# Optimization experiments

Hardware: AMD Instinct MI355X
Metric: run time of the kernel (lower is better)

Reference implementation:

```python
import jax, jax.numpy as jnp
import numpy as np

B, INPUT_DIM, OUTPUT_DIM, Z_DIM = 32, 2048, 2048, 64
NNZ = 209715


def setup_inputs() -> dict:
    key = jax.random.key(0)
    k_x, k_z, k_w, k_b = jax.random.split(key, 4)
    x = jax.random.normal(k_x, (B, INPUT_DIM), dtype=jnp.float32)
    z = jax.random.normal(k_z, (B, Z_DIM), dtype=jnp.float32)
    W_net = jax.random.normal(k_w, (Z_DIM, NNZ), dtype=jnp.float32) * 0.02
    b_net = jax.random.normal(k_b, (NNZ,), dtype=jnp.float32) * 0.02
    # unique nonzero positions of output_matrix [INPUT_DIM, OUTPUT_DIM]
    rng = np.random.default_rng(0)
    lin = rng.choice(INPUT_DIM * OUTPUT_DIM, size=NNZ, replace=False)
    in_idx = jnp.asarray(lin // OUTPUT_DIM, dtype=jnp.int32)   # rows  -> input dim
    out_idx = jnp.asarray(lin % OUTPUT_DIM, dtype=jnp.int32)   # cols  -> output dim
    return {"x": x, "z": z, "W_net": W_net, "b_net": b_net,
            "in_idx": in_idx, "out_idx": out_idx}


def reference(x, z, W_net, b_net, in_idx, out_idx):
    # hypernetwork: net(z) -> [B, NNZ] matrix entries
    mat_entity = z @ W_net + b_net                      # [B, NNZ]
    # scatter into zero-filled dense matrix: mat[:, out_idx, in_idx] = entries
    mat = jnp.zeros((x.shape[0], OUTPUT_DIM, INPUT_DIM), dtype=x.dtype)
    mat = mat.at[:, out_idx, in_idx].set(mat_entity)    # [B, O, I]
    # batched matvec
    return jnp.einsum('boi,bi->bo', mat, x)             # [B, O]
```

## Files before the change

kernel.cpp:

```cpp
#include <hip/hip_runtime.h>
#include <hip/hip_bf16.h>

#define BATCH   32
#define IN_DIM  2048
#define OUT_DIM 2048
#define ZDIM    64
#define NNZ     209715
#define CAP     160
#define TILES   ((NNZ + 15) / 16)
#define TPW     2
#define CWAVES  ((TILES + TPW - 1) / TPW)
#define CBLOCKS ((CWAVES + 3) / 4)
#define NBLK    ((NNZ + 1023) / 1024)

typedef __attribute__((ext_vector_type(8))) short bf16x8;
typedef __attribute__((ext_vector_type(4))) float f32x4;

#define OFF_XT   0
#define OFF_ZBF  262144
#define OFF_CNT  270336
#define OFF_BH   278528
#define OFF_ROW  2375680
#define OFF_E    3214592
#define B_WS_NEEDED (OFF_E + (size_t)OUT_DIM * CAP * BATCH * 2)

__device__ __forceinline__ short f2bf(float f) {
    unsigned u = __float_as_uint(f);
    u += 0x7fffu + ((u >> 16) & 1u);
    return (short)(u >> 16);
}

__global__ __launch_bounds__(1024) void hist_prep(
    const int* __restrict__ out_idx, const float* __restrict__ x,
    const float* __restrict__ z, int* __restrict__ bh,
    float* __restrict__ xT, short* __restrict__ zbf)
{
    __shared__ int lh[OUT_DIM];
    const int t = threadIdx.x, blk = blockIdx.x;
    lh[t] = 0; lh[t + 1024] = 0;
    __syncthreads();
    const int gid = blk * 1024 + t;
    if (gid < BATCH * IN_DIM) {
        const int b = gid >> 11, i = gid & 2047;
        xT[i * BATCH + b] = x[gid];
        if (gid < BATCH * ZDIM) zbf[gid] = f2bf(z[gid]);
    }
    if (gid < NNZ) atomicAdd(&lh[out_idx[gid]], 1);
    __syncthreads();
    bh[t * 256 + blk]          = lh[t];
    bh[(t + 1024) * 256 + blk] = lh[t + 1024];
}

__global__ __launch_bounds__(256) void colscan(
    int* __restrict__ bh, int* __restrict__ cnt)
{
    const int o    = blockIdx.x * 4 + (threadIdx.x >> 6);
    const int lane = threadIdx.x & 63;
    const int i0   = lane * 4;
    int4 v = *reinterpret_cast<int4*>(bh + o * 256 + i0);
    const int a = (i0 + 0 < NBLK) ? v.x : 0;
    const int b = (i0 + 1 < NBLK) ? v.y : 0;
    const int c = (i0 + 2 < NBLK) ? v.z : 0;
    const int d = (i0 + 3 < NBLK) ? v.w : 0;
    const int s1 = a + b, s2 = s1 + c, tot = s2 + d;
    int inc = tot;
    #pragma unroll
    for (int t = 1; t < 64; t <<= 1) {
        const int n = __shfl_up(inc, t);
        if (lane >= t) inc += n;
    }
    const int exc = inc - tot;
    int4 w; w.x = exc; w.y = exc + a; w.z = exc + s1; w.w = exc + s2;
    *reinterpret_cast<int4*>(bh + o * 256 + i0) = w;
    if (lane == 63) cnt[o] = inc;
}

__global__ __launch_bounds__(1024) void slot_blk(
    const int* __restrict__ out_idx, const int* __restrict__ bh,
    int* __restrict__ rowOf)
{
    __shared__ int lh[OUT_DIM];
    const int t = threadIdx.x, blk = blockIdx.x;
    lh[t] = 0; lh[t + 1024] = 0;
    __syncthreads();
    const int k = blk * 1024 + t;
    if (k < NNZ) {
        const int oi  = out_idx[k];
        const int r   = atomicAdd(&lh[oi], 1);
        const int pos = bh[oi * 256 + blk] + r;
        rowOf[k] = (pos < CAP) ? oi * CAP + pos : -1;
    }
}

__global__ __launch_bounds__(256, 4) void compute_mfma(
    const short* __restrict__ zbf, const float* __restrict__ W,
    const float* __restrict__ bn, const int* __restrict__ in_idx,
    const int* __restrict__ rowOf, const float* __restrict__ xT,
    short* __restrict__ E)
{
    const int lane = threadIdx.x & 63;
    const int m    = lane & 15;
    const int hi   = lane >> 4;
    const int wid  = blockIdx.x * 4 + (threadIdx.x >> 6);
    const int t0   = wid * TPW;
    if (t0 >= TILES) return;

    bf16x8 zf[2][2];
    #pragma unroll
    for (int bt = 0; bt < 2; ++bt)
        #pragma unroll
        for (int jt = 0; jt < 2; ++jt)
            zf[bt][jt] = *reinterpret_cast<const bf16x8*>(
                zbf + (bt * 16 + m) * ZDIM + jt * 32 + hi * 8);

    int rowL[2] = {-1, -1}, iiL[2] = {0, 0};
    float bnL[2] = {0.f, 0.f};
    #pragma unroll
    for (int tt = 0; tt < TPW; ++tt) {
        const int t = t0 + tt;
        if (t < TILES && lane < 16) {
            const int kk = t * 16 + lane;
            if (kk < NNZ) { rowL[tt] = rowOf[kk]; iiL[tt] = in_idx[kk]; bnL[tt] = bn[kk]; }
        }
    }

    float wv[2][16];
    #pragma unroll
    for (int tt = 0; tt < TPW; ++tt) {
        const int t  = (t0 + tt < TILES) ? (t0 + tt) : (TILES - 1);
        const int kA = (t * 16 + m < NNZ) ? (t * 16 + m) : (NNZ - 1);
        const float* wp = W + (size_t)(hi * 8) * NNZ + kA;
        #pragma unroll
        for (int e = 0; e < 8; ++e) wv[tt][e]     = wp[(size_t)e * NNZ];
        #pragma unroll
        for (int e = 0; e < 8; ++e) wv[tt][8 + e] = wp[(size_t)(32 + e) * NNZ];
    }

    int   row_[2][4];
    float x0_[2][4], x1_[2][4];
    #pragma unroll
    for (int tt = 0; tt < TPW; ++tt)
        #pragma unroll
        for (int r = 0; r < 4; ++r) {
            const int src = hi * 4 + r;
            row_[tt][r] = __shfl(rowL[tt], src);
            const int ii = __shfl(iiL[tt], src);
            x0_[tt][r] = xT[ii * BATCH + m];
            x1_[tt][r] = xT[ii * BATCH + 16 + m];
        }

    #pragma unroll
    for (int tt = 0; tt < TPW; ++tt) {
        union { bf16x8 v; short s[8]; } a0, a1;
        #pragma unroll
        for (int e = 0; e < 8; ++e) { a0.s[e] = f2bf(wv[tt][e]); a1.s[e] = f2bf(wv[tt][8 + e]); }

        f32x4 acc0 = {0.f, 0.f, 0.f, 0.f};
        f32x4 acc1 = {0.f, 0.f, 0.f, 0.f};
        acc0 = __builtin_amdgcn_mfma_f32_16x16x32_bf16(a0.v, zf[0][0], acc0, 0, 0, 0);
        acc0 = __builtin_amdgcn_mfma_f32_16x16x32_bf16(a1.v, zf[0][1], acc0, 0, 0, 0);
        acc1 = __builtin_amdgcn_mfma_f32_16x16x32_bf16(a0.v, zf[1][0], acc1, 0, 0, 0);
        acc1 = __builtin_amdgcn_mfma_f32_16x16x32_bf16(a1.v, zf[1][1], acc1, 0, 0, 0);

        #pragma unroll
        for (int r = 0; r < 4; ++r) {
            const int row = row_[tt][r];
            if (row >= 0) {
                const float bb = __shfl(bnL[tt], hi * 4 + r);
                short* Ep = E + (size_t)row * BATCH;
                Ep[m]      = f2bf((acc0[r] + bb) * x0_[tt][r]);
                Ep[16 + m] = f2bf((acc1[r] + bb) * x1_[tt][r]);
            }
        }
    }
}

__global__ __launch_bounds__(256) void reduce_bf16(
    const short* __restrict__ E, const int* __restrict__ cnt,
    float* __restrict__ out)
{
    const int o    = blockIdx.x * 4 + (threadIdx.x >> 6);
    const int lane = threadIdx.x & 63;
    const int r  = lane >> 2;
    const int bg = lane & 3;
    const int s = o * CAP;
    int c = cnt[o]; if (c > CAP) c = CAP;
    const int e = s + c;

    float acc[8];
    #pragma unroll
    for (int q = 0; q < 8; ++q) acc[q] = 0.f;

    for (int p = s + r; p < e; p += 16) {
        const uint4 v = *reinterpret_cast<const uint4*>(E + (size_t)p * BATCH + bg * 8);
        const unsigned u[4] = {v.x, v.y, v.z, v.w};
        #pragma unroll
        for (int q = 0; q < 4; ++q) {
            acc[2 * q]     += __uint_as_float((u[q] & 0xFFFFu) << 16);
            acc[2 * q + 1] += __uint_as_float(u[q] & 0xFFFF0000u);
        }
    }

    #pragma unroll
    for (int d = 4; d < 64; d <<= 1)
        #pragma unroll
        for (int q = 0; q < 8; ++q)
            acc[q] += __shfl_xor(acc[q], d);

    if (lane < 4) {
        #pragma unroll
        for (int q = 0; q < 8; ++q)
            out[(bg * 8 + q) * OUT_DIM + o] = acc[q];
    }
}

__global__ __launch_bounds__(256) void hyper_scatter_kernel(
    const float* __restrict__ x, const float* __restrict__ z,
    const float* __restrict__ W, const float* __restrict__ bn,
    const int* __restrict__ in_idx, const int* __restrict__ out_idx,
    float* __restrict__ out)
{
    __shared__ float zs[BATCH * ZDIM];
    const int tid = threadIdx.x;
    {
        const float4* zg  = reinterpret_cast<const float4*>(z);
        float4*       zsv = reinterpret_cast<float4*>(zs);
        zsv[tid]       = zg[tid];
        zsv[tid + 256] = zg[tid + 256];
    }
    __syncthreads();
    const int k = blockIdx.x * 256 + tid;
    if (k >= NNZ) return;
    float w[ZDIM];
    #pragma unroll
    for (int j = 0; j < ZDIM; ++j) w[j] = W[(size_t)j * NNZ + k];
    const float bk = bn[k];
    const int ii = in_idx[k], oi = out_idx[k];
    const float4* zv = reinterpret_cast<const float4*>(zs);
    #pragma unroll
    for (int b = 0; b < BATCH; ++b) {
        float e = bk;
        #pragma unroll
        for (int j4 = 0; j4 < ZDIM / 4; ++j4) {
            const float4 zz = zv[b * (ZDIM / 4) + j4];
            e = fmaf(zz.x, w[j4 * 4 + 0], e);
            e = fmaf(zz.y, w[j4 * 4 + 1], e);
            e = fmaf(zz.z, w[j4 * 4 + 2], e);
            e = fmaf(zz.w, w[j4 * 4 + 3], e);
        }
        atomicAdd(&out[b * OUT_DIM + oi], e * x[b * IN_DIM + ii]);
    }
}

extern "C" void kernel_launch(void* const* d_in, const int* in_sizes, int n_in,
                              void* d_out, int out_size, void* d_ws, size_t ws_size,
                              hipStream_t stream) {
    const float* x       = (const float*)d_in[0];
    const float* z       = (const float*)d_in[1];
    const float* W       = (const float*)d_in[2];
    const float* bn      = (const float*)d_in[3];
    const int*   in_idx  = (const int*)d_in[4];
    const int*   out_idx = (const int*)d_in[5];
    float*       out     = (float*)d_out;
    char*        ws      = (char*)d_ws;

    if (ws_size >= B_WS_NEEDED) {
        float* xT    = (float*)(ws + OFF_XT);
        short* zbf   = (short*)(ws + OFF_ZBF);
        int*   cnt   = (int*)(ws + OFF_CNT);
        int*   bh    = (int*)(ws + OFF_BH);
        int*   rowOf = (int*)(ws + OFF_ROW);
        short* E     = (short*)(ws + OFF_E);

        hist_prep<<<NBLK, 1024, 0, stream>>>(out_idx, x, z, bh, xT, zbf);
        colscan  <<<OUT_DIM / 4, 256, 0, stream>>>(bh, cnt);
        slot_blk <<<NBLK, 1024, 0, stream>>>(out_idx, bh, rowOf);
        compute_mfma<<<CBLOCKS, 256, 0, stream>>>(zbf, W, bn, in_idx, rowOf, xT, E);
        reduce_bf16 <<<OUT_DIM / 4, 256, 0, stream>>>(E, cnt, out);
    } else {
        hipMemsetAsync(out, 0, (size_t)BATCH * OUT_DIM * sizeof(float), stream);
        const int grid = (NNZ + 255) / 256;
        hyper_scatter_kernel<<<grid, 256, 0, stream>>>(x, z, W, bn, in_idx, out_idx, out);
    }
}
```

Before: 42.78 us.

## Replace histogram/scan slot assignment with global atomic slot counters in compute

Removes the three-kernel histogram, column-scan and slot-assignment pipeline and instead assigns each nonzero's bucket slot with a global atomicAdd on a per-output counter inside the MFMA compute kernel. A small prep kernel zeroes the counters alongside the x transpose and z conversion. This cuts two kernel launches and the bh/rowOf memory traffic, at the cost of contended global atomics on 2048 counters. Slot order becomes nondeterministic, which changes the bf16 summation order in the reduce.

```diff
diff --git a/kernel.cpp b/kernel.cpp
--- a/kernel.cpp
+++ b/kernel.cpp
@@ -11,17 +11,14 @@
 #define TPW     2
 #define CWAVES  ((TILES + TPW - 1) / TPW)
 #define CBLOCKS ((CWAVES + 3) / 4)
-#define NBLK    ((NNZ + 1023) / 1024)
 
 typedef __attribute__((ext_vector_type(8))) short bf16x8;
 typedef __attribute__((ext_vector_type(4))) float f32x4;
 
 #define OFF_XT   0
 #define OFF_ZBF  262144
-#define OFF_CNT  270336
-#define OFF_BH   278528
-#define OFF_ROW  2375680
-#define OFF_E    3214592
+#define OFF_CUR  266240
+#define OFF_E    274432
 #define B_WS_NEEDED (OFF_E + (size_t)OUT_DIM * CAP * BATCH * 2)
 
 __device__ __forceinline__ short f2bf(float f) {
@@ -30,73 +27,23 @@
     return (short)(u >> 16);
 }
 
-__global__ __launch_bounds__(1024) void hist_prep(
-    const int* __restrict__ out_idx, const float* __restrict__ x,
-    const float* __restrict__ z, int* __restrict__ bh,
-    float* __restrict__ xT, short* __restrict__ zbf)
-{
-    __shared__ int lh[OUT_DIM];
-    const int t = threadIdx.x, blk = blockIdx.x;
-    lh[t] = 0; lh[t + 1024] = 0;
-    __syncthreads();
-    const int gid = blk * 1024 + t;
-    if (gid < BATCH * IN_DIM) {
-        const int b = gid >> 11, i = gid & 2047;
-        xT[i * BATCH + b] = x[gid];
-        if (gid < BATCH * ZDIM) zbf[gid] = f2bf(z[gid]);
-    }
-    if (gid < NNZ) atomicAdd(&lh[out_idx[gid]], 1);
-    __syncthreads();
-    bh[t * 256 + blk]          = lh[t];
-    bh[(t + 1024) * 256 + blk] = lh[t + 1024];
-}
-
-__global__ __launch_bounds__(256) void colscan(
-    int* __restrict__ bh, int* __restrict__ cnt)
-{
-    const int o    = blockIdx.x * 4 + (threadIdx.x >> 6);
-    const int lane = threadIdx.x & 63;
-    const int i0   = lane * 4;
-    int4 v = *reinterpret_cast<int4*>(bh + o * 256 + i0);
-    const int a = (i0 + 0 < NBLK) ? v.x : 0;
-    const int b = (i0 + 1 < NBLK) ? v.y : 0;
-    const int c = (i0 + 2 < NBLK) ? v.z : 0;
-    const int d = (i0 + 3 < NBLK) ? v.w : 0;
-    const int s1 = a + b, s2 = s1 + c, tot = s2 + d;
-    int inc = tot;
-    #pragma unroll
-    for (int t = 1; t < 64; t <<= 1) {
-        const int n = __shfl_up(inc, t);
-        if (lane >= t) inc += n;
-    }
-    const int exc = inc - tot;
-    int4 w; w.x = exc; w.y = exc + a; w.z = exc + s1; w.w = exc + s2;
-    *reinterpret_cast<int4*>(bh + o * 256 + i0) = w;
-    if (lane == 63) cnt[o] = inc;
-}
-
-__global__ __launch_bounds__(1024) void slot_blk(
-    const int* __restrict__ out_idx, const int* __restrict__ bh,
-    int* __restrict__ rowOf)
-{
-    __shared__ int lh[OUT_DIM];
-    const int t = threadIdx.x, blk = blockIdx.x;
-    lh[t] = 0; lh[t + 1024] = 0;
-    __syncthreads();
-    const int k = blk * 1024 + t;
-    if (k < NNZ) {
-        const int oi  = out_idx[k];
-        const int r   = atomicAdd(&lh[oi], 1);
-        const int pos = bh[oi * 256 + blk] + r;
-        rowOf[k] = (pos < CAP) ? oi * CAP + pos : -1;
-    }
+__global__ __launch_bounds__(256) void prep_x(
+    const float* __restrict__ x, const float* __restrict__ z,
+    float* __restrict__ xT, short* __restrict__ zbf, int* __restrict__ cur)
+{
+    const int idx = blockIdx.x * 256 + threadIdx.x;
+    const int b = idx >> 11;
+    const int i = idx & 2047;
+    xT[i * BATCH + b] = x[idx];
+    if (idx < BATCH * ZDIM) zbf[idx] = f2bf(z[idx]);
+    if (idx < OUT_DIM)      cur[idx] = 0;
 }
 
 __global__ __launch_bounds__(256, 4) void compute_mfma(
     const short* __restrict__ zbf, const float* __restrict__ W,
     const float* __restrict__ bn, const int* __restrict__ in_idx,
-    const int* __restrict__ rowOf, const float* __restrict__ xT,
-    short* __restrict__ E)
+    const int* __restrict__ out_idx, const float* __restrict__ xT,
+    int* __restrict__ cur, short* __restrict__ E)
 {
     const int lane = threadIdx.x & 63;
     const int m    = lane & 15;
@@ -120,7 +67,13 @@
         const int t = t0 + tt;
         if (t < TILES && lane < 16) {
             const int kk = t * 16 + lane;
-            if (kk < NNZ) { rowL[tt] = rowOf[kk]; iiL[tt] = in_idx[kk]; bnL[tt] = bn[kk]; }
+            if (kk < NNZ) {
+                iiL[tt] = in_idx[kk];
+                bnL[tt] = bn[kk];
+                const int oi = out_idx[kk];
+                const int p  = atomicAdd(&cur[oi], 1);
+                rowL[tt] = (p < CAP) ? oi * CAP + p : -1;
+            }
         }
     }
 
@@ -136,15 +89,12 @@
         for (int e = 0; e < 8; ++e) wv[tt][8 + e] = wp[(size_t)(32 + e) * NNZ];
     }
 
-    int   row_[2][4];
     float x0_[2][4], x1_[2][4];
     #pragma unroll
     for (int tt = 0; tt < TPW; ++tt)
         #pragma unroll
         for (int r = 0; r < 4; ++r) {
-            const int src = hi * 4 + r;
-            row_[tt][r] = __shfl(rowL[tt], src);
-            const int ii = __shfl(iiL[tt], src);
+            const int ii = __shfl(iiL[tt], hi * 4 + r);
             x0_[tt][r] = xT[ii * BATCH + m];
             x1_[tt][r] = xT[ii * BATCH + 16 + m];
         }
@@ -164,9 +114,10 @@
 
         #pragma unroll
         for (int r = 0; r < 4; ++r) {
-            const int row = row_[tt][r];
+            const int src = hi * 4 + r;
+            const int row = __shfl(rowL[tt], src);
             if (row >= 0) {
-                const float bb = __shfl(bnL[tt], hi * 4 + r);
+                const float bb = __shfl(bnL[tt], src);
                 short* Ep = E + (size_t)row * BATCH;
                 Ep[m]      = f2bf((acc0[r] + bb) * x0_[tt][r]);
                 Ep[16 + m] = f2bf((acc1[r] + bb) * x1_[tt][r]);
@@ -265,18 +216,14 @@
     char*        ws      = (char*)d_ws;
 
     if (ws_size >= B_WS_NEEDED) {
-        float* xT    = (float*)(ws + OFF_XT);
-        short* zbf   = (short*)(ws + OFF_ZBF);
-        int*   cnt   = (int*)(ws + OFF_CNT);
-        int*   bh    = (int*)(ws + OFF_BH);
-        int*   rowOf = (int*)(ws + OFF_ROW);
-        short* E     = (short*)(ws + OFF_E);
-
-        hist_prep<<<NBLK, 1024, 0, stream>>>(out_idx, x, z, bh, xT, zbf);
-        colscan  <<<OUT_DIM / 4, 256, 0, stream>>>(bh, cnt);
-        slot_blk <<<NBLK, 1024, 0, stream>>>(out_idx, bh, rowOf);
-        compute_mfma<<<CBLOCKS, 256, 0, stream>>>(zbf, W, bn, in_idx, rowOf, xT, E);
-        reduce_bf16 <<<OUT_DIM / 4, 256, 0, stream>>>(E, cnt, out);
+        float* xT  = (float*)(ws + OFF_XT);
+        short* zbf = (short*)(ws + OFF_ZBF);
+        int*   cur = (int*)(ws + OFF_CUR);
+        short* E   = (short*)(ws + OFF_E);
+
+        prep_x      <<<(BATCH * IN_DIM) / 256, 256, 0, stream>>>(x, z, xT, zbf, cur);
+        compute_mfma<<<CBLOCKS, 256, 0, stream>>>(zbf, W, bn, in_idx, out_idx, xT, cur, E);
+        reduce_bf16 <<<OUT_DIM / 4, 256, 0, stream>>>(E, cur, out);
     } else {
         hipMemsetAsync(out, 0, (size_t)BATCH * OUT_DIM * sizeof(float), stream);
         const int grid = (NNZ + 255) / 256;
```

Result: slower. 55.63 us (+30.0%).

## Fuse slot assignment into histogram pass and drop slot_blk kernel

Applied to the files above, without the earlier changes.

The histogram kernel now records each nonzero's local rank within its block together with its output index in a packed word. The compute kernel rebuilds the destination row by adding that rank to the scanned block offset, so the separate slot_blk kernel, which re-read out_idx and redid the shared atomics, is gone. This saves one kernel launch and one pass over the index data. In exchange the compute kernel does an extra dependent gather from bh, and the packing relies on the atomic rank being the same one used for the histogram.

```diff
diff --git a/kernel.cpp b/kernel.cpp
--- a/kernel.cpp
+++ b/kernel.cpp
@@ -16,12 +16,12 @@
 typedef __attribute__((ext_vector_type(8))) short bf16x8;
 typedef __attribute__((ext_vector_type(4))) float f32x4;
 
-#define OFF_XT   0
-#define OFF_ZBF  262144
-#define OFF_CNT  270336
-#define OFF_BH   278528
-#define OFF_ROW  2375680
-#define OFF_E    3214592
+#define OFF_XT    0
+#define OFF_ZBF   262144
+#define OFF_CNT   266240
+#define OFF_BH    274432
+#define OFF_COMBO 2371584
+#define OFF_E     3210496
 #define B_WS_NEEDED (OFF_E + (size_t)OUT_DIM * CAP * BATCH * 2)
 
 __device__ __forceinline__ short f2bf(float f) {
@@ -33,7 +33,7 @@
 __global__ __launch_bounds__(1024) void hist_prep(
     const int* __restrict__ out_idx, const float* __restrict__ x,
     const float* __restrict__ z, int* __restrict__ bh,
-    float* __restrict__ xT, short* __restrict__ zbf)
+    int* __restrict__ combo, float* __restrict__ xT, short* __restrict__ zbf)
 {
     __shared__ int lh[OUT_DIM];
     const int t = threadIdx.x, blk = blockIdx.x;
@@ -45,7 +45,11 @@
         xT[i * BATCH + b] = x[gid];
         if (gid < BATCH * ZDIM) zbf[gid] = f2bf(z[gid]);
     }
-    if (gid < NNZ) atomicAdd(&lh[out_idx[gid]], 1);
+    if (gid < NNZ) {
+        const int oi = out_idx[gid];
+        const int r  = atomicAdd(&lh[oi], 1);
+        combo[gid] = (r << 11) | oi;
+    }
     __syncthreads();
     bh[t * 256 + blk]          = lh[t];
     bh[(t + 1024) * 256 + blk] = lh[t + 1024];
@@ -75,28 +79,11 @@
     if (lane == 63) cnt[o] = inc;
 }
 
-__global__ __launch_bounds__(1024) void slot_blk(
-    const int* __restrict__ out_idx, const int* __restrict__ bh,
-    int* __restrict__ rowOf)
-{
-    __shared__ int lh[OUT_DIM];
-    const int t = threadIdx.x, blk = blockIdx.x;
-    lh[t] = 0; lh[t + 1024] = 0;
-    __syncthreads();
-    const int k = blk * 1024 + t;
-    if (k < NNZ) {
-        const int oi  = out_idx[k];
-        const int r   = atomicAdd(&lh[oi], 1);
-        const int pos = bh[oi * 256 + blk] + r;
-        rowOf[k] = (pos < CAP) ? oi * CAP + pos : -1;
-    }
-}
-
 __global__ __launch_bounds__(256, 4) void compute_mfma(
     const short* __restrict__ zbf, const float* __restrict__ W,
     const float* __restrict__ bn, const int* __restrict__ in_idx,
-    const int* __restrict__ rowOf, const float* __restrict__ xT,
-    short* __restrict__ E)
+    const int* __restrict__ combo, const int* __restrict__ bh,
+    const float* __restrict__ xT, short* __restrict__ E)
 {
     const int lane = threadIdx.x & 63;
     const int m    = lane & 15;
@@ -120,7 +107,14 @@
         const int t = t0 + tt;
         if (t < TILES && lane < 16) {
             const int kk = t * 16 + lane;
-            if (kk < NNZ) { rowL[tt] = rowOf[kk]; iiL[tt] = in_idx[kk]; bnL[tt] = bn[kk]; }
+            if (kk < NNZ) {
+                iiL[tt] = in_idx[kk];
+                bnL[tt] = bn[kk];
+                const int cb  = combo[kk];
+                const int oi  = cb & 2047;
+                const int pos = bh[oi * 256 + (kk >> 10)] + (cb >> 11);
+                rowL[tt] = (pos < CAP) ? oi * CAP + pos : -1;
+            }
         }
     }
 
@@ -136,15 +130,12 @@
         for (int e = 0; e < 8; ++e) wv[tt][8 + e] = wp[(size_t)(32 + e) * NNZ];
     }
 
-    int   row_[2][4];
     float x0_[2][4], x1_[2][4];
     #pragma unroll
     for (int tt = 0; tt < TPW; ++tt)
         #pragma unroll
         for (int r = 0; r < 4; ++r) {
-            const int src = hi * 4 + r;
-            row_[tt][r] = __shfl(rowL[tt], src);
-            const int ii = __shfl(iiL[tt], src);
+            const int ii = __shfl(iiL[tt], hi * 4 + r);
             x0_[tt][r] = xT[ii * BATCH + m];
             x1_[tt][r] = xT[ii * BATCH + 16 + m];
         }
@@ -164,9 +155,10 @@
 
         #pragma unroll
         for (int r = 0; r < 4; ++r) {
-            const int row = row_[tt][r];
+            const int src = hi * 4 + r;
+            const int row = __shfl(rowL[tt], src);
             if (row >= 0) {
-                const float bb = __shfl(bnL[tt], hi * 4 + r);
+                const float bb = __shfl(bnL[tt], src);
                 short* Ep = E + (size_t)row * BATCH;
                 Ep[m]      = f2bf((acc0[r] + bb) * x0_[tt][r]);
                 Ep[16 + m] = f2bf((acc1[r] + bb) * x1_[tt][r]);
@@ -269,13 +261,12 @@
         short* zbf   = (short*)(ws + OFF_ZBF);
         int*   cnt   = (int*)(ws + OFF_CNT);
         int*   bh    = (int*)(ws + OFF_BH);
-        int*   rowOf = (int*)(ws + OFF_ROW);
+        int*   combo = (int*)(ws + OFF_COMBO);
         short* E     = (short*)(ws + OFF_E);
 
-        hist_prep<<<NBLK, 1024, 0, stream>>>(out_idx, x, z, bh, xT, zbf);
+        hist_prep<<<NBLK, 1024, 0, stream>>>(out_idx, x, z, bh, combo, xT, zbf);
         colscan  <<<OUT_DIM / 4, 256, 0, stream>>>(bh, cnt);
-        slot_blk <<<NBLK, 1024, 0, stream>>>(out_idx, bh, rowOf);
-        compute_mfma<<<CBLOCKS, 256, 0, stream>>>(zbf, W, bn, in_idx, rowOf, xT, E);
+        compute_mfma<<<CBLOCKS, 256, 0, stream>>>(zbf, W, bn, in_idx, combo, bh, xT, E);
         reduce_bf16 <<<OUT_DIM / 4, 256, 0, stream>>>(E, cnt, out);
     } else {
         hipMemsetAsync(out, 0, (size_t)BATCH * OUT_DIM * sizeof(float), stream);
```

Result: faster. 41.23 us (-3.6%).
